# Kernel tuning notes

Hardware: AMD Instinct MI355X
Metric: run time of the kernel (lower is better)

The kernel has to match this reference:

```python
import jax, jax.numpy as jnp
import numpy as np

D_MODEL = 1024
D_STATE = 16
LN_EPS = 1e-5


def setup_inputs() -> dict:
    key = jax.random.key(0)
    ks = jax.random.split(key, 10)
    B, L, D, N = 4, 1024, D_MODEL, D_STATE
    s = lambda fan_in: 1.0 / np.sqrt(fan_in)
    x_in = jax.random.normal(ks[0], (B, L, D), dtype=jnp.float32)
    W_in = jax.random.uniform(ks[1], (D, 2 * D), jnp.float32, -s(D), s(D))
    W_x = jax.random.uniform(ks[2], (D, D + 2 * N), jnp.float32, -s(D), s(D))
    W_dt = jax.random.uniform(ks[3], (D, D), jnp.float32, -s(D), s(D))
    b_dt = jax.random.uniform(ks[4], (D,), jnp.float32, -4.0, -1.0)
    A_log = jnp.tile(jnp.log(jnp.arange(1, N + 1, dtype=jnp.float32))[None, :], (D, 1))
    D_param = jnp.ones((D,), dtype=jnp.float32)
    W_out = jax.random.uniform(ks[5], (D, D), jnp.float32, -s(D), s(D))
    ln_g = jnp.ones((D,), dtype=jnp.float32)
    ln_b = jnp.zeros((D,), dtype=jnp.float32)
    return {"x_in": x_in, "W_in": W_in, "W_x": W_x, "W_dt": W_dt, "b_dt": b_dt,
            "A_log": A_log, "D_param": D_param, "W_out": W_out, "ln_g": ln_g, "ln_b": ln_b}


def reference(x_in, W_in, W_x, W_dt, b_dt, A_log, D_param, W_out, ln_g, ln_b):
    B, L, D = x_in.shape
    N = A_log.shape[1]
    xz = x_in @ W_in                       # [B,L,2D]
    x, z = xz[..., :D], xz[..., D:]
    proj = x @ W_x                         # [B,L,D+2N]
    delta_raw = proj[..., :D]
    B_ssm = proj[..., D:D + N]
    C_ssm = proj[..., D + N:]
    delta = jax.nn.softplus(delta_raw @ W_dt + b_dt)   # [B,L,D]
    A = -jnp.exp(A_log)                    # [D,N]
    dA = jnp.exp(jnp.einsum('bld,dn->bldn', delta, A))      # [B,L,D,N]
    dBx = jnp.einsum('bld,bln->bldn', delta * x, B_ssm)      # dB * x, fused

    def step(h, inp):
        dA_t, dBx_t, C_t = inp             # [B,D,N],[B,D,N],[B,N]
        h = dA_t * h + dBx_t
        y_t = jnp.einsum('bdn,bn->bd', h, C_t)
        return h, y_t

    h0 = jnp.zeros((B, D, N), dtype=x.dtype)
    xs = (jnp.moveaxis(dA, 1, 0), jnp.moveaxis(dBx, 1, 0), jnp.moveaxis(C_ssm, 1, 0))
    _, ys = jax.lax.scan(step, h0, xs)     # ys: [L,B,D]
    y = jnp.moveaxis(ys, 0, 1) + x * D_param
    y = (y * jax.nn.silu(z)) @ W_out
    res = y + x_in
    mu = jnp.mean(res, axis=-1, keepdims=True)
    var = jnp.var(res, axis=-1, keepdims=True)
    return (res - mu) * jax.lax.rsqrt(var + LN_EPS) * ln_g + ln_b
```

## Files before the change

### kernel.cpp

```cpp
#include <hip/hip_runtime.h>

#define D_MODEL 1024
#define D_STATE 16
#define M_ROWS  4096
#define SEQ_L   1024
#define NSEG    64
#define LSEG    16

typedef __bf16 bf16x8 __attribute__((ext_vector_type(8)));
typedef float  f32x4  __attribute__((ext_vector_type(4)));

__device__ __forceinline__ unsigned short f2bf(float f) {
  unsigned int u = __builtin_bit_cast(unsigned int, f);
  u += 0x7fffu + ((u >> 16) & 1u);
  return (unsigned short)(u >> 16);
}
__device__ __forceinline__ float bf2f(unsigned short b) {
  unsigned int u = ((unsigned int)b) << 16;
  return __builtin_bit_cast(float, u);
}
__device__ __forceinline__ float load_elem(const void* p, size_t i, int isbf) {
  if (isbf) return bf2f(((const unsigned short*)p)[i]);
  return ((const float*)p)[i];
}

__device__ __forceinline__ int is_bf16(const void* x_in) {
  unsigned int v = ((const unsigned short*)x_in)[2 * (threadIdx.x & 63)];
  unsigned int e = (v >> 7) & 0xFFu;
  unsigned long long m = __ballot(e >= 100u && e <= 135u);
  return __popcll(m) >= 32;
}

__device__ __forceinline__ void gload16(const void* g, void* l) {
  typedef const __attribute__((address_space(1))) unsigned int GU;
  typedef __attribute__((address_space(3))) unsigned int LU;
  __builtin_amdgcn_global_load_lds((GU*)(unsigned long long)g,
                                   (LU*)(unsigned int)(unsigned long long)l,
                                   16, 0, 0);
}

__global__ void prep_kernel(const void* __restrict__ x_in, unsigned short* __restrict__ x_b,
                            const void* __restrict__ W_in, const void* __restrict__ W_x,
                            const void* __restrict__ W_dt, const void* __restrict__ W_out,
                            unsigned short* __restrict__ wx_raw,
                            unsigned short* __restrict__ wt_in, unsigned short* __restrict__ wt_xbc,
                            unsigned short* __restrict__ wt_dt, unsigned short* __restrict__ wt_out,
                            const void* b_dt, const void* A_log, const void* Dp,
                            const void* ln_g, const void* ln_b,
                            float* o_bdt, float* o_a2, float* o_dp,
                            float* o_lng, float* o_lnb) {
  __shared__ float tile[32][33];
  const int isbf = is_bf16(x_in);
  const int bid = blockIdx.x;
  const int tid = threadIdx.x;
  if (bid < 2048 || (bid >= 2128 && bid < 2656)) {
    const void* src; unsigned short* dst; int c;
    if (bid < 2048) { src = x_in; dst = x_b; c = bid * 256 + tid; }
    else { src = W_x; dst = wx_raw; c = (bid - 2128) * 256 + tid; }
    if (isbf) {
      ((uint4*)dst)[c] = ((const uint4*)src)[c];
    } else {
      float4 a = ((const float4*)src)[2 * c];
      float4 b = ((const float4*)src)[2 * c + 1];
      uint4 p;
      p.x = (unsigned int)f2bf(a.x) | ((unsigned int)f2bf(a.y) << 16);
      p.y = (unsigned int)f2bf(a.z) | ((unsigned int)f2bf(a.w) << 16);
      p.z = (unsigned int)f2bf(b.x) | ((unsigned int)f2bf(b.y) << 16);
      p.w = (unsigned int)f2bf(b.z) | ((unsigned int)f2bf(b.w) << 16);
      ((uint4*)dst)[c] = p;
    }
  } else if (bid < 2128) {
    int g = (bid - 2048) * 256 + tid;
    if (g < 1024)              o_bdt[g]          = load_elem(b_dt, g, isbf);
    else if (g < 17408) {
      float v = load_elem(A_log, g - 1024, isbf);
      o_a2[g - 1024] = -expf(v) * 1.4426950408889634f;
    }
    else if (g < 18432)        o_dp[g - 17408]   = load_elem(Dp, g - 17408, isbf);
    else if (g < 19456)        o_lng[g - 18432]  = load_elem(ln_g, g - 18432, isbf);
    else                       o_lnb[g - 19456]  = load_elem(ln_b, g - 19456, isbf);
  } else {
    int t = bid - 2656;
    const void* src; unsigned short* dst; int ncols, col0, bxx, byy;
    if (t < 2048)      { src = W_in;  dst = wt_in;  ncols = 2048; col0 = 0;
                         bxx = t & 63; byy = t >> 6; }
    else if (t < 2176) { t -= 2048; src = W_x; dst = wt_xbc; ncols = 1056; col0 = 1024;
                         bxx = t & 3; byy = t >> 2; }
    else if (t < 3200) { t -= 2176; src = W_dt; dst = wt_dt; ncols = 1024; col0 = 0;
                         bxx = t & 31; byy = t >> 5; }
    else               { t -= 3200; src = W_out; dst = wt_out; ncols = 1024; col0 = 0;
                         bxx = t & 31; byy = t >> 5; }
    int tx = tid & 31, ty = tid >> 5;
    int n0 = col0 + bxx * 32, k0 = byy * 32;
    #pragma unroll
    for (int r = 0; r < 4; ++r) {
      int k = k0 + ty + r * 8;
      int n = n0 + tx;
      float v = (n < ncols) ? load_elem(src, (size_t)k * ncols + n, isbf) : 0.f;
      tile[ty + r * 8][tx] = v;
    }
    __syncthreads();
    #pragma unroll
    for (int r = 0; r < 4; ++r) {
      int n = n0 + ty + r * 8;
      int k = k0 + tx;
      dst[(size_t)(n - col0) * 1024 + k] = f2bf(tile[tx][ty + r * 8]);
    }
  }
}

template<int MODE>
__global__ __launch_bounds__(256, MODE == 1 ? 4 : 6) void gemm_bf(
    const unsigned short* __restrict__ A, const unsigned short* __restrict__ Bt, int ldb,
    void* __restrict__ o0, void* __restrict__ o1, void* __restrict__ o2,
    float* __restrict__ o3, float* __restrict__ o4,
    const float* __restrict__ aux, const void* __restrict__ auxv,
    const unsigned short* __restrict__ A_u, const unsigned short* __restrict__ B_u,
    int ldb_u, void* __restrict__ o_u) {
  constexpr int BN = (MODE == 1) ? 128 : 64;
  constexpr int NJ = BN / 32;
  constexpr int BW = BN / 4;
  __shared__ __align__(16) unsigned short a_lds[3][64 * 32];
  __shared__ __align__(16) unsigned short b_lds[3][BN * 32];
  const int isbf = (MODE == 4) ? is_bf16(auxv) : 0;
  const int tid = threadIdx.x;
  const int wave = tid >> 6, lane = tid & 63;
  const int wr = (wave >> 1) * 32, wc = (wave & 1) * (BN / 2);
  const int lrow = lane & 15, quad = lane >> 4;

  const int bx = blockIdx.x, by = blockIdx.y;

  int m0, n0, ldbl = ldb;
  const unsigned short* Asrc = A;
  const unsigned short* Bsrc = Bt;
  bool isU = false;
  if (MODE == 1 && bx >= 64) {
    isU = true;
    int u = (bx - 64) * 16 + by;
    m0 = (u >> 3) * 64; n0 = (u & 7) * 128;
    Asrc = A_u; Bsrc = B_u; ldbl = ldb_u;
  } else {
    m0 = bx * 64; n0 = by * BN;
    if (MODE == 2 && n0 >= 1024) { Bsrc = (const unsigned short*)o2; n0 -= 1024; }
  }
  const int nout = (MODE == 2 && Bsrc == (const unsigned short*)o2) ? n0 + 1024 : n0;

  const int sc = (lane & 3) ^ ((lane >> 3) & 3);
  const unsigned short* gA  = Asrc + (size_t)(m0 + wave * 16 + (lane >> 2)) * 1024 + sc * 8;
  const unsigned short* gB  = Bsrc + (size_t)(n0 + wave * BW + (lane >> 2)) * ldbl + sc * 8;
  const unsigned short* gB2 = gB + (size_t)16 * ldbl;
  const int q2 = quad ^ ((lrow >> 1) & 3);

  f32x4 acc[2][NJ];
  #pragma unroll
  for (int i = 0; i < 2; ++i)
    #pragma unroll
    for (int j = 0; j < NJ; ++j)
      #pragma unroll
      for (int r = 0; r < 4; ++r) acc[i][j][r] = 0.f;

  auto issue = [&](int k) {
    unsigned short* ab = a_lds[k % 3] + wave * 16 * 32;
    unsigned short* bb = b_lds[k % 3] + wave * BW * 32;
    gload16(gA + k * 32, ab);
    gload16(gB + k * 32, bb);
    if constexpr (MODE == 1) gload16(gB2 + k * 32, bb + 16 * 32);
  };
  auto compute = [&](int k) {
    const unsigned short* ard = a_lds[k % 3] + (wr + lrow) * 32 + q2 * 8;
    const unsigned short* brd = b_lds[k % 3] + (wc + lrow) * 32 + q2 * 8;
    bf16x8 af[2], bfr[NJ];
    #pragma unroll
    for (int i = 0; i < 2; ++i) af[i] = *(const bf16x8*)(ard + i * 16 * 32);
    #pragma unroll
    for (int j = 0; j < NJ; ++j) bfr[j] = *(const bf16x8*)(brd + j * 16 * 32);
    #pragma unroll
    for (int i = 0; i < 2; ++i)
      #pragma unroll
      for (int j = 0; j < NJ; ++j)
        acc[i][j] = __builtin_amdgcn_mfma_f32_16x16x32_bf16(af[i], bfr[j], acc[i][j], 0, 0, 0);
  };

  issue(0);
  issue(1);
  #pragma unroll
  for (int k = 0; k < 31; ++k) {
    if constexpr (MODE == 1)
      asm volatile("s_waitcnt vmcnt(3)" ::: "memory");
    else
      asm volatile("s_waitcnt vmcnt(2)" ::: "memory");
    __builtin_amdgcn_s_barrier();
    if (k + 2 < 32) issue(k + 2);
    compute(k);
  }
  asm volatile("s_waitcnt vmcnt(0)" ::: "memory");
  __builtin_amdgcn_s_barrier();
  compute(31);

  #pragma unroll
  for (int i = 0; i < 2; ++i) {
    #pragma unroll
    for (int jj = 0; jj < NJ; ++jj) {
      #pragma unroll
      for (int r = 0; r < 4; ++r) {
        int m = m0 + wr + i * 16 + quad * 4 + r;
        int n = nout + wc + jj * 16 + lrow;
        float v = acc[i][jj][r];
        if (MODE == 1) {
          if (isU) {
            ((unsigned short*)o_u)[(size_t)m * 1024 + n] = f2bf(v);
          } else if (n < 1024) {
            ((unsigned short*)o0)[(size_t)m * 1024 + n] = f2bf(v);
          } else {
            float sig = 1.f / (1.f + expf(-v));
            ((unsigned short*)o1)[(size_t)m * 1024 + (n - 1024)] = f2bf(v * sig);
          }
        } else if (MODE == 2) {
          if (n < 1024) {
            float t = v + aux[n];
            float sp = (t > 20.f) ? t : log1pf(expf(t));
            ((unsigned short*)o0)[(size_t)m * 1024 + n] = f2bf(sp);
          }
          else if (n < 1040)  o3[(size_t)m * D_STATE + (n - 1024)] = v;
          else if (n < 1056)  o4[(size_t)m * D_STATE + (n - 1040)] = v;
        } else {
          ((float*)o0)[(size_t)m * 1024 + n] =
              v + load_elem(auxv, (size_t)m * 1024 + n, isbf);
        }
      }
    }
  }
}

template<int PHASE>
__global__ __launch_bounds__(256) void scan_phase(
    const unsigned short* __restrict__ dl_bf, const unsigned short* __restrict__ x_bf,
    const unsigned short* __restrict__ z_bf, const float* __restrict__ Bs,
    const float* __restrict__ Cs, const float* __restrict__ A2g,
    const float* __restrict__ Dpar, const float* __restrict__ hinit,
    float* __restrict__ Hout, float* __restrict__ sdout,
    unsigned short* __restrict__ g) {
  __shared__ float4 bsh[LSEG][4];
  __shared__ float4 csh[LSEG][4];
  const int tid = threadIdx.x;
  const int bid = blockIdx.x;
  const int seg = bid >> 4;
  const int b = (bid >> 2) & 3;
  const int dc = bid & 3;
  const int d = dc * 256 + tid;
  const int t0 = seg * LSEG;
  const int bd = b * D_MODEL + d;

  if (tid < LSEG * 4) {
    int r = tid >> 2, q = tid & 3;
    size_t src = ((size_t)b * SEQ_L + t0 + r) * 4 + q;
    bsh[r][q] = ((const float4*)Bs)[src];
    if (PHASE == 1) csh[r][q] = ((const float4*)Cs)[src];
  }

  float A2r[16];
  {
    const float4* a4 = (const float4*)(A2g + (size_t)d * 16);
    #pragma unroll
    for (int q = 0; q < 4; ++q) {
      float4 v = a4[q];
      A2r[4*q] = v.x; A2r[4*q+1] = v.y; A2r[4*q+2] = v.z; A2r[4*q+3] = v.w;
    }
  }
  float h[16];
  if (PHASE == 1) {
    const float4* h4 = (const float4*)(hinit + (((size_t)seg * 4096) + bd) * 16);
    #pragma unroll
    for (int q = 0; q < 4; ++q) {
      float4 v = h4[q];
      h[4*q] = v.x; h[4*q+1] = v.y; h[4*q+2] = v.z; h[4*q+3] = v.w;
    }
  } else {
    #pragma unroll
    for (int n = 0; n < 16; ++n) h[n] = 0.f;
  }
  const float Dpd = (PHASE == 1) ? Dpar[d] : 0.f;
  float sd = 0.f;
  const size_t base = ((size_t)b * SEQ_L + t0) * D_MODEL + d;
  __syncthreads();

  unsigned short dreg[2][8], xreg[2][8], zreg[2][8];
  #pragma unroll
  for (int t = 0; t < 8; ++t) {
    size_t o = base + (size_t)t * D_MODEL;
    dreg[0][t] = dl_bf[o]; xreg[0][t] = x_bf[o];
    if (PHASE == 1) zreg[0][t] = z_bf[o];
  }
  #pragma unroll
  for (int c = 0; c < LSEG / 8; ++c) {
    const int cur = c & 1, nxt = cur ^ 1;
    if (c < LSEG / 8 - 1) {
      #pragma unroll
      for (int t = 0; t < 8; ++t) {
        size_t o = base + (size_t)((c + 1) * 8 + t) * D_MODEL;
        dreg[nxt][t] = dl_bf[o]; xreg[nxt][t] = x_bf[o];
        if (PHASE == 1) zreg[nxt][t] = z_bf[o];
      }
    }
    #pragma unroll
    for (int t = 0; t < 8; ++t) {
      const int tt = c * 8 + t;
      float dl = bf2f(dreg[cur][t]);
      float xx = bf2f(xreg[cur][t]);
      float dx = dl * xx;
      sd += dl;
      float4 b0 = bsh[tt][0], b1 = bsh[tt][1], b2 = bsh[tt][2], b3 = bsh[tt][3];
      float bb[16] = {b0.x,b0.y,b0.z,b0.w, b1.x,b1.y,b1.z,b1.w,
                      b2.x,b2.y,b2.z,b2.w, b3.x,b3.y,b3.z,b3.w};
      if (PHASE == 0) {
        #pragma unroll
        for (int n = 0; n < 16; ++n) {
          float dA = exp2f(dl * A2r[n]);
          h[n] = fmaf(dA, h[n], dx * bb[n]);
        }
      } else {
        float4 c0 = csh[tt][0], c1 = csh[tt][1], c2 = csh[tt][2], c3 = csh[tt][3];
        float cc[16] = {c0.x,c0.y,c0.z,c0.w, c1.x,c1.y,c1.z,c1.w,
                        c2.x,c2.y,c2.z,c2.w, c3.x,c3.y,c3.z,c3.w};
        float y = 0.f;
        #pragma unroll
        for (int n = 0; n < 16; ++n) {
          float dA = exp2f(dl * A2r[n]);
          h[n] = fmaf(dA, h[n], dx * bb[n]);
          y = fmaf(h[n], cc[n], y);
        }
        float zz = bf2f(zreg[cur][t]);
        g[base + (size_t)tt * D_MODEL] = f2bf(fmaf(xx, Dpd, y) * zz);
      }
    }
  }
  if (PHASE == 0) {
    float4* ho = (float4*)(Hout + (((size_t)seg * 4096) + bd) * 16);
    #pragma unroll
    for (int q = 0; q < 4; ++q)
      ho[q] = make_float4(h[4*q], h[4*q+1], h[4*q+2], h[4*q+3]);
    sdout[(size_t)seg * 4096 + bd] = sd;
  }
}

__global__ __launch_bounds__(256) void scan_phaseB(
    const float* __restrict__ H, const float* __restrict__ sdelta,
    const float* __restrict__ A2g, float* __restrict__ hinit) {
  int gidx = blockIdx.x * 256 + threadIdx.x;
  int bd = gidx >> 4, n = gidx & 15;
  float A2 = A2g[(size_t)(bd & (D_MODEL - 1)) * 16 + n];
  float hp = 0.f;
  #pragma unroll 8
  for (int s = 0; s < NSEG; ++s) {
    size_t idx = ((size_t)s * 4096 + bd) * 16 + n;
    hinit[idx] = hp;
    float P = exp2f(A2 * sdelta[(size_t)s * 4096 + bd]);
    hp = fmaf(P, hp, H[idx]);
  }
}

__global__ __launch_bounds__(256) void ln_kernel(const float* __restrict__ res,
    const float* __restrict__ lng, const float* __restrict__ lnb,
    void* __restrict__ out, const void* __restrict__ x_in) {
  const int isbf = is_bf16(x_in);
  int row = blockIdx.x, tid = threadIdx.x;
  const float4* r4 = (const float4*)(res + (size_t)row * D_MODEL);
  float4 v = r4[tid];
  float s = v.x + v.y + v.z + v.w;
  float q = v.x * v.x + v.y * v.y + v.z * v.z + v.w * v.w;
  #pragma unroll
  for (int m = 1; m < 64; m <<= 1) { s += __shfl_xor(s, m); q += __shfl_xor(q, m); }
  __shared__ float ss[4], qs[4];
  int w = tid >> 6;
  if ((tid & 63) == 0) { ss[w] = s; qs[w] = q; }
  __syncthreads();
  s = ss[0] + ss[1] + ss[2] + ss[3];
  q = qs[0] + qs[1] + qs[2] + qs[3];
  float mu = s * (1.f / D_MODEL);
  float var = q * (1.f / D_MODEL) - mu * mu;
  float rstd = rsqrtf(var + 1e-5f);
  float4 gg = ((const float4*)lng)[tid];
  float4 bb = ((const float4*)lnb)[tid];
  float o0 = (v.x - mu) * rstd * gg.x + bb.x;
  float o1 = (v.y - mu) * rstd * gg.y + bb.y;
  float o2 = (v.z - mu) * rstd * gg.z + bb.z;
  float o3 = (v.w - mu) * rstd * gg.w + bb.w;
  if (isbf) {
    ushort4 pv;
    pv.x = f2bf(o0); pv.y = f2bf(o1); pv.z = f2bf(o2); pv.w = f2bf(o3);
    ((ushort4*)out)[(size_t)row * 256 + tid] = pv;
  } else {
    ((float4*)out)[(size_t)row * 256 + tid] = make_float4(o0, o1, o2, o3);
  }
}

extern "C" void kernel_launch(void* const* d_in, const int* in_sizes, int n_in,
                              void* d_out, int out_size, void* d_ws, size_t ws_size,
                              hipStream_t stream) {
  (void)in_sizes; (void)n_in; (void)out_size; (void)ws_size;
  const void* x_in  = d_in[0];
  const void* W_in  = d_in[1];
  const void* W_x   = d_in[2];
  const void* W_dt  = d_in[3];
  const void* b_dt  = d_in[4];
  const void* A_log = d_in[5];
  const void* D_par = d_in[6];
  const void* W_out = d_in[7];
  const void* ln_g  = d_in[8];
  const void* ln_b  = d_in[9];

  char* ws = (char*)d_ws;
  size_t off = 0;
  auto alloc = [&](size_t bytes) -> void* {
    void* p = ws + off;
    off += (bytes + 255) & ~(size_t)255;
    return p;
  };
  unsigned short* x_in_b  = (unsigned short*)alloc((size_t)M_ROWS * D_MODEL * 2);
  unsigned short* wx_raw  = (unsigned short*)alloc((size_t)1024 * 1056 * 2);
  float* bdt_f            = (float*)alloc(1024 * 4);
  float* a2_f             = (float*)alloc(16384 * 4);
  float* dp_f             = (float*)alloc(1024 * 4);
  float* lng_f            = (float*)alloc(1024 * 4);
  float* lnb_f            = (float*)alloc(1024 * 4);
  unsigned short* wt_in   = (unsigned short*)alloc((size_t)2048 * 1024 * 2);
  unsigned short* wt_xbc  = (unsigned short*)alloc((size_t)128 * 1024 * 2);
  unsigned short* wt_dt   = (unsigned short*)alloc((size_t)1024 * 1024 * 2);
  unsigned short* wt_out  = (unsigned short*)alloc((size_t)1024 * 1024 * 2);
  unsigned short* U_bf    = (unsigned short*)alloc((size_t)1024 * 1024 * 2);
  unsigned short* x_bf    = (unsigned short*)alloc((size_t)M_ROWS * D_MODEL * 2);
  unsigned short* s_bf    = (unsigned short*)alloc((size_t)M_ROWS * D_MODEL * 2);
  unsigned short* delta_bf= (unsigned short*)alloc((size_t)M_ROWS * D_MODEL * 2);
  unsigned short* g_bf    = (unsigned short*)alloc((size_t)M_ROWS * D_MODEL * 2);
  float* bssm_f           = (float*)alloc((size_t)M_ROWS * D_STATE * 4);
  float* cssm_f           = (float*)alloc((size_t)M_ROWS * D_STATE * 4);
  float* H_f              = (float*)alloc((size_t)NSEG * 4096 * 16 * 4);
  float* hinit_f          = (float*)alloc((size_t)NSEG * 4096 * 16 * 4);
  float* sdelta_f         = (float*)alloc((size_t)NSEG * 4096 * 4);
  float* res_f = (float*)x_bf;

  prep_kernel<<<6880, 256, 0, stream>>>(x_in, x_in_b, W_in, W_x, W_dt, W_out,
                                        wx_raw, wt_in, wt_xbc, wt_dt, wt_out,
                                        b_dt, A_log, D_par, ln_g, ln_b,
                                        bdt_f, a2_f, dp_f, lng_f, lnb_f);

  gemm_bf<1><<<dim3(72, 16), 256, 0, stream>>>(x_in_b, wt_in, 1024,
      x_bf, s_bf, nullptr, nullptr, nullptr, nullptr, nullptr,
      wt_dt, wx_raw, 1056, U_bf);

  gemm_bf<2><<<dim3(64, 17), 256, 0, stream>>>(x_bf, U_bf, 1024,
      delta_bf, nullptr, wt_xbc, bssm_f, cssm_f, bdt_f, nullptr,
      nullptr, nullptr, 0, nullptr);

  scan_phase<0><<<1024, 256, 0, stream>>>(delta_bf, x_bf, nullptr, bssm_f, nullptr,
                                          a2_f, nullptr, nullptr, H_f, sdelta_f, nullptr);
  scan_phaseB<<<256, 256, 0, stream>>>(H_f, sdelta_f, a2_f, hinit_f);
  scan_phase<1><<<1024, 256, 0, stream>>>(delta_bf, x_bf, s_bf, bssm_f, cssm_f,
                                          a2_f, dp_f, hinit_f, nullptr, nullptr, g_bf);

  gemm_bf<4><<<dim3(64, 16), 256, 0, stream>>>(g_bf, wt_out, 1024,
      res_f, nullptr, nullptr, nullptr, nullptr, nullptr, x_in,
      nullptr, nullptr, 0, nullptr);

  ln_kernel<<<4096, 256, 0, stream>>>(res_f, lng_f, lnb_f, d_out, x_in);
}
```

Baseline: 252.1 us.

## Fuse three-phase chunked scan into one cooperative kernel with grid syncs

Replaces the three scan launches (per-segment local scan, cross-segment carry propagation, final scan with output gating) with a single cooperative kernel that separates the phases with grid.sync. Delta and x values are kept in registers between the first and third phase, so they are not reloaded, and two kernel launch boundaries disappear. In exchange the kernel relies on all 1024 blocks being co-resident (launch bounds of 4 blocks per CU) and pays for grid-wide barriers. If the cooperative launch fails it falls back to the original three kernels.

```diff
diff --git a/kernel.cpp b/kernel.cpp
--- a/kernel.cpp
+++ b/kernel.cpp
@@ -1,4 +1,7 @@
 #include <hip/hip_runtime.h>
+#include <hip/hip_cooperative_groups.h>
+
+namespace cg = cooperative_groups;
 
 #define D_MODEL 1024
 #define D_STATE 16
@@ -228,6 +231,130 @@
               v + load_elem(auxv, (size_t)m * 1024 + n, isbf);
         }
       }
+    }
+  }
+}
+
+__global__ __launch_bounds__(256, 4) void scan_fused(
+    const unsigned short* __restrict__ dl_bf, const unsigned short* __restrict__ x_bf,
+    const unsigned short* __restrict__ z_bf, const float* __restrict__ Bs,
+    const float* __restrict__ Cs, const float* __restrict__ A2g,
+    const float* __restrict__ Dpar, float* __restrict__ H,
+    float* __restrict__ sdelta, float* __restrict__ hinit,
+    unsigned short* __restrict__ g) {
+  cg::grid_group grid = cg::this_grid();
+  __shared__ float4 bsh[LSEG][4];
+  __shared__ float4 csh[LSEG][4];
+  const int tid = threadIdx.x;
+  const int bid = blockIdx.x;
+  const int seg = bid >> 4;
+  const int b = (bid >> 2) & 3;
+  const int dc = bid & 3;
+  const int d = dc * 256 + tid;
+  const int t0 = seg * LSEG;
+  const int bd = b * D_MODEL + d;
+  const size_t base = ((size_t)b * SEQ_L + t0) * D_MODEL + d;
+
+  if (tid < LSEG * 4) {
+    int r = tid >> 2, q = tid & 3;
+    size_t src = ((size_t)b * SEQ_L + t0 + r) * 4 + q;
+    bsh[r][q] = ((const float4*)Bs)[src];
+    csh[r][q] = ((const float4*)Cs)[src];
+  }
+
+  float A2r[16];
+  {
+    const float4* a4 = (const float4*)(A2g + (size_t)d * 16);
+    #pragma unroll
+    for (int q = 0; q < 4; ++q) {
+      float4 v = a4[q];
+      A2r[4*q] = v.x; A2r[4*q+1] = v.y; A2r[4*q+2] = v.z; A2r[4*q+3] = v.w;
+    }
+  }
+  unsigned short dreg[LSEG], xreg[LSEG];
+  #pragma unroll
+  for (int t = 0; t < LSEG; ++t) {
+    size_t o = base + (size_t)t * D_MODEL;
+    dreg[t] = dl_bf[o]; xreg[t] = x_bf[o];
+  }
+  __syncthreads();
+
+  {
+    float h[16];
+    #pragma unroll
+    for (int n = 0; n < 16; ++n) h[n] = 0.f;
+    float sd = 0.f;
+    #pragma unroll
+    for (int t = 0; t < LSEG; ++t) {
+      float dl = bf2f(dreg[t]);
+      float dx = dl * bf2f(xreg[t]);
+      sd += dl;
+      float4 b0 = bsh[t][0], b1 = bsh[t][1], b2 = bsh[t][2], b3 = bsh[t][3];
+      float bb[16] = {b0.x,b0.y,b0.z,b0.w, b1.x,b1.y,b1.z,b1.w,
+                      b2.x,b2.y,b2.z,b2.w, b3.x,b3.y,b3.z,b3.w};
+      #pragma unroll
+      for (int n = 0; n < 16; ++n) {
+        float dA = exp2f(dl * A2r[n]);
+        h[n] = fmaf(dA, h[n], dx * bb[n]);
+      }
+    }
+    float4* ho = (float4*)(H + (((size_t)seg * 4096) + bd) * 16);
+    #pragma unroll
+    for (int q = 0; q < 4; ++q)
+      ho[q] = make_float4(h[4*q], h[4*q+1], h[4*q+2], h[4*q+3]);
+    sdelta[(size_t)seg * 4096 + bd] = sd;
+  }
+  __threadfence();
+  grid.sync();
+
+  if (bid < 256) {
+    int gidx = bid * 256 + tid;
+    int bd2 = gidx >> 4, n2 = gidx & 15;
+    float A2 = A2g[(size_t)(bd2 & (D_MODEL - 1)) * 16 + n2];
+    float hp = 0.f;
+    #pragma unroll 8
+    for (int s = 0; s < NSEG; ++s) {
+      size_t idx = ((size_t)s * 4096 + bd2) * 16 + n2;
+      hinit[idx] = hp;
+      float P = exp2f(A2 * sdelta[(size_t)s * 4096 + bd2]);
+      hp = fmaf(P, hp, H[idx]);
+    }
+  }
+  __threadfence();
+  grid.sync();
+
+  {
+    float h[16];
+    const float4* h4 = (const float4*)(hinit + (((size_t)seg * 4096) + bd) * 16);
+    #pragma unroll
+    for (int q = 0; q < 4; ++q) {
+      float4 v = h4[q];
+      h[4*q] = v.x; h[4*q+1] = v.y; h[4*q+2] = v.z; h[4*q+3] = v.w;
+    }
+    const float Dpd = Dpar[d];
+    unsigned short zreg[LSEG];
+    #pragma unroll
+    for (int t = 0; t < LSEG; ++t) zreg[t] = z_bf[base + (size_t)t * D_MODEL];
+    #pragma unroll
+    for (int t = 0; t < LSEG; ++t) {
+      float dl = bf2f(dreg[t]);
+      float xx = bf2f(xreg[t]);
+      float dx = dl * xx;
+      float4 b0 = bsh[t][0], b1 = bsh[t][1], b2 = bsh[t][2], b3 = bsh[t][3];
+      float bb[16] = {b0.x,b0.y,b0.z,b0.w, b1.x,b1.y,b1.z,b1.w,
+                      b2.x,b2.y,b2.z,b2.w, b3.x,b3.y,b3.z,b3.w};
+      float4 c0 = csh[t][0], c1 = csh[t][1], c2 = csh[t][2], c3 = csh[t][3];
+      float cc[16] = {c0.x,c0.y,c0.z,c0.w, c1.x,c1.y,c1.z,c1.w,
+                      c2.x,c2.y,c2.z,c2.w, c3.x,c3.y,c3.z,c3.w};
+      float y = 0.f;
+      #pragma unroll
+      for (int n = 0; n < 16; ++n) {
+        float dA = exp2f(dl * A2r[n]);
+        h[n] = fmaf(dA, h[n], dx * bb[n]);
+        y = fmaf(h[n], cc[n], y);
+      }
+      float zz = bf2f(zreg[t]);
+      g[base + (size_t)t * D_MODEL] = f2bf(fmaf(xx, Dpd, y) * zz);
     }
   }
 }
@@ -452,11 +579,32 @@
       delta_bf, nullptr, wt_xbc, bssm_f, cssm_f, bdt_f, nullptr,
       nullptr, nullptr, 0, nullptr);
 
-  scan_phase<0><<<1024, 256, 0, stream>>>(delta_bf, x_bf, nullptr, bssm_f, nullptr,
-                                          a2_f, nullptr, nullptr, H_f, sdelta_f, nullptr);
-  scan_phaseB<<<256, 256, 0, stream>>>(H_f, sdelta_f, a2_f, hinit_f);
-  scan_phase<1><<<1024, 256, 0, stream>>>(delta_bf, x_bf, s_bf, bssm_f, cssm_f,
-                                          a2_f, dp_f, hinit_f, nullptr, nullptr, g_bf);
+  {
+    const unsigned short* a_dl = delta_bf;
+    const unsigned short* a_x  = x_bf;
+    const unsigned short* a_z  = s_bf;
+    const float* a_B = bssm_f;
+    const float* a_C = cssm_f;
+    const float* a_A2 = a2_f;
+    const float* a_Dp = dp_f;
+    float* a_H = H_f;
+    float* a_sd = sdelta_f;
+    float* a_hi = hinit_f;
+    unsigned short* a_g = g_bf;
+    void* kargs[] = {(void*)&a_dl, (void*)&a_x, (void*)&a_z, (void*)&a_B, (void*)&a_C,
+                     (void*)&a_A2, (void*)&a_Dp, (void*)&a_H, (void*)&a_sd,
+                     (void*)&a_hi, (void*)&a_g};
+    hipError_t ce = hipLaunchCooperativeKernel((void*)scan_fused, dim3(1024), dim3(256),
+                                               kargs, 0, stream);
+    if (ce != hipSuccess) {
+      (void)hipGetLastError();
+      scan_phase<0><<<1024, 256, 0, stream>>>(delta_bf, x_bf, nullptr, bssm_f, nullptr,
+                                              a2_f, nullptr, nullptr, H_f, sdelta_f, nullptr);
+      scan_phaseB<<<256, 256, 0, stream>>>(H_f, sdelta_f, a2_f, hinit_f);
+      scan_phase<1><<<1024, 256, 0, stream>>>(delta_bf, x_bf, s_bf, bssm_f, cssm_f,
+                                              a2_f, dp_f, hinit_f, nullptr, nullptr, g_bf);
+    }
+  }
 
   gemm_bf<4><<<dim3(64, 16), 256, 0, stream>>>(g_bf, wt_out, 1024,
       res_f, nullptr, nullptr, nullptr, nullptr, nullptr, x_in,
```

Measured after the change: 873.8 us. 3.47x slower.

## Use 512-thread blocks with eight waves for the input-projection GEMM

Applied to the files above, without the earlier changes.

The MODE 1 GEMM (64x128 tile) now launches 512 threads, giving eight waves that each compute a 16x64 sub-tile instead of four waves computing 32x64. The global-to-LDS load split is reworked so the first four waves load A and all eight load one 16-row B slice, with per-wave vmcnt waits adjusted to match. The aim is more waves in flight to hide latency and fewer accumulators per wave, at the cost of less register-level reuse of A and B fragments and more barrier participants.

```diff
diff --git a/kernel.cpp b/kernel.cpp
--- a/kernel.cpp
+++ b/kernel.cpp
@@ -110,7 +110,7 @@
 }
 
 template<int MODE>
-__global__ __launch_bounds__(256, MODE == 1 ? 4 : 6) void gemm_bf(
+__global__ __launch_bounds__(MODE == 1 ? 512 : 256, MODE == 1 ? 8 : 6) void gemm_bf(
     const unsigned short* __restrict__ A, const unsigned short* __restrict__ Bt, int ldb,
     void* __restrict__ o0, void* __restrict__ o1, void* __restrict__ o2,
     float* __restrict__ o3, float* __restrict__ o4,
@@ -119,13 +119,14 @@
     int ldb_u, void* __restrict__ o_u) {
   constexpr int BN = (MODE == 1) ? 128 : 64;
   constexpr int NJ = BN / 32;
-  constexpr int BW = BN / 4;
+  constexpr int MI = (MODE == 1) ? 1 : 2;
   __shared__ __align__(16) unsigned short a_lds[3][64 * 32];
   __shared__ __align__(16) unsigned short b_lds[3][BN * 32];
   const int isbf = (MODE == 4) ? is_bf16(auxv) : 0;
   const int tid = threadIdx.x;
   const int wave = tid >> 6, lane = tid & 63;
-  const int wr = (wave >> 1) * 32, wc = (wave & 1) * (BN / 2);
+  const int wr = (wave >> 1) * (MI * 16);
+  const int wc = (wave & 1) * (BN / 2);
   const int lrow = lane & 15, quad = lane >> 4;
 
   const int bx = blockIdx.x, by = blockIdx.y;
@@ -146,36 +147,36 @@
   const int nout = (MODE == 2 && Bsrc == (const unsigned short*)o2) ? n0 + 1024 : n0;
 
   const int sc = (lane & 3) ^ ((lane >> 3) & 3);
-  const unsigned short* gA  = Asrc + (size_t)(m0 + wave * 16 + (lane >> 2)) * 1024 + sc * 8;
-  const unsigned short* gB  = Bsrc + (size_t)(n0 + wave * BW + (lane >> 2)) * ldbl + sc * 8;
-  const unsigned short* gB2 = gB + (size_t)16 * ldbl;
+  const unsigned short* gA = Asrc + (size_t)(m0 + (wave & 3) * 16 + (lane >> 2)) * 1024 + sc * 8;
+  const unsigned short* gB = Bsrc + (size_t)(n0 + wave * 16 + (lane >> 2)) * ldbl + sc * 8;
   const int q2 = quad ^ ((lrow >> 1) & 3);
 
-  f32x4 acc[2][NJ];
-  #pragma unroll
-  for (int i = 0; i < 2; ++i)
+  f32x4 acc[MI][NJ];
+  #pragma unroll
+  for (int i = 0; i < MI; ++i)
     #pragma unroll
     for (int j = 0; j < NJ; ++j)
       #pragma unroll
       for (int r = 0; r < 4; ++r) acc[i][j][r] = 0.f;
 
   auto issue = [&](int k) {
-    unsigned short* ab = a_lds[k % 3] + wave * 16 * 32;
-    unsigned short* bb = b_lds[k % 3] + wave * BW * 32;
-    gload16(gA + k * 32, ab);
+    if (MODE != 1 || wave < 4) {
+      unsigned short* ab = a_lds[k % 3] + (wave & 3) * 16 * 32;
+      gload16(gA + k * 32, ab);
+    }
+    unsigned short* bb = b_lds[k % 3] + wave * 16 * 32;
     gload16(gB + k * 32, bb);
-    if constexpr (MODE == 1) gload16(gB2 + k * 32, bb + 16 * 32);
   };
   auto compute = [&](int k) {
     const unsigned short* ard = a_lds[k % 3] + (wr + lrow) * 32 + q2 * 8;
     const unsigned short* brd = b_lds[k % 3] + (wc + lrow) * 32 + q2 * 8;
-    bf16x8 af[2], bfr[NJ];
-    #pragma unroll
-    for (int i = 0; i < 2; ++i) af[i] = *(const bf16x8*)(ard + i * 16 * 32);
+    bf16x8 af[MI], bfr[NJ];
+    #pragma unroll
+    for (int i = 0; i < MI; ++i) af[i] = *(const bf16x8*)(ard + i * 16 * 32);
     #pragma unroll
     for (int j = 0; j < NJ; ++j) bfr[j] = *(const bf16x8*)(brd + j * 16 * 32);
     #pragma unroll
-    for (int i = 0; i < 2; ++i)
+    for (int i = 0; i < MI; ++i)
       #pragma unroll
       for (int j = 0; j < NJ; ++j)
         acc[i][j] = __builtin_amdgcn_mfma_f32_16x16x32_bf16(af[i], bfr[j], acc[i][j], 0, 0, 0);
@@ -185,10 +186,12 @@
   issue(1);
   #pragma unroll
   for (int k = 0; k < 31; ++k) {
-    if constexpr (MODE == 1)
-      asm volatile("s_waitcnt vmcnt(3)" ::: "memory");
-    else
+    if constexpr (MODE == 1) {
+      if (wave < 4) asm volatile("s_waitcnt vmcnt(2)" ::: "memory");
+      else          asm volatile("s_waitcnt vmcnt(1)" ::: "memory");
+    } else {
       asm volatile("s_waitcnt vmcnt(2)" ::: "memory");
+    }
     __builtin_amdgcn_s_barrier();
     if (k + 2 < 32) issue(k + 2);
     compute(k);
@@ -198,7 +201,7 @@
   compute(31);
 
   #pragma unroll
-  for (int i = 0; i < 2; ++i) {
+  for (int i = 0; i < MI; ++i) {
     #pragma unroll
     for (int jj = 0; jj < NJ; ++jj) {
       #pragma unroll
@@ -444,7 +447,7 @@
                                         b_dt, A_log, D_par, ln_g, ln_b,
                                         bdt_f, a2_f, dp_f, lng_f, lnb_f);
 
-  gemm_bf<1><<<dim3(72, 16), 256, 0, stream>>>(x_in_b, wt_in, 1024,
+  gemm_bf<1><<<dim3(72, 16), 512, 0, stream>>>(x_in_b, wt_in, 1024,
       x_bf, s_bf, nullptr, nullptr, nullptr, nullptr, nullptr,
       wt_dt, wx_raw, 1056, U_bf);
 
```

Measured after the change: 252.9 us. Within noise of the previous version (+0.3%).
